# Kernel tuning notes

Measured on AMD Instinct MI355X. Metric: run time of the kernel, lower is better.

The kernel has to match this reference:

```python
import jax, jax.numpy as jnp
import numpy as np

L, B, S, D, H, FF = 6, 4, 1024, 256, 8, 128
DH = D // H
EPS = 1e-5


def _ln(x, w, b):
    m = x.mean(-1, keepdims=True)
    v = ((x - m) ** 2).mean(-1, keepdims=True)
    return (x - m) / jnp.sqrt(v + EPS) * w + b


def setup_inputs() -> dict:
    key = jax.random.key(0)
    ks = jax.random.split(key, 6)
    s = lambda k, shape: jax.random.normal(k, shape, jnp.float32) * 0.02
    return {
        "x": jax.random.normal(ks[0], (B, S, D), jnp.float32),
        "ln1_w": jnp.ones((L, D), jnp.float32),
        "ln1_b": jnp.zeros((L, D), jnp.float32),
        "wqkv": s(ks[1], (L, D, 3 * D)),   # qkv_linear, bias=False
        "wout": s(ks[2], (L, D, D)),       # out_linear, bias=False
        "ln2_w": jnp.ones((L, D), jnp.float32),
        "ln2_b": jnp.zeros((L, D), jnp.float32),
        "w1": s(ks[3], (L, D, 2 * FF)),    # Linear(d_model, 2*ff)
        "b1": jnp.zeros((L, 2 * FF), jnp.float32),
        "w2": s(ks[4], (L, FF, D)),        # Linear(ff, d_model)
        "b2": jnp.zeros((L, D), jnp.float32),
    }


def reference(x, ln1_w, ln1_b, wqkv, wout, ln2_w, ln2_b, w1, b1, w2, b2):
    attn_weights_list = []
    scale = 1.0 / jnp.sqrt(jnp.float32(DH))
    for i in range(L):
        # --- pre-norm multi-head attention ---
        xn = _ln(x, ln1_w[i], ln1_b[i])
        qkv = xn @ wqkv[i]                       # [B,S,3D]
        q, k, v = jnp.split(qkv, 3, axis=-1)
        rs = lambda t: t.reshape(B, S, H, DH).transpose(0, 2, 1, 3)  # b h s d
        q, k, v = rs(q), rs(k), rs(v)
        logits = jnp.einsum('bhid,bhjd->bhij', q, k) * scale
        aw = jax.nn.softmax(logits, axis=-1)     # [B,H,S,S] (dropout=0, eval)
        attn_weights_list.append(aw)
        o = jnp.einsum('bhij,bhjd->bhid', aw, v)
        o = o.transpose(0, 2, 1, 3).reshape(B, S, D) @ wout[i]
        x = x + o
        # --- pre-norm GEGLU FFN ---
        h = _ln(x, ln2_w[i], ln2_b[i]) @ w1[i] + b1[i]   # [B,S,2*FF]
        a, g = jnp.split(h, 2, axis=-1)
        x = x + (a * jax.nn.gelu(g, approximate=False)) @ w2[i] + b2[i]
    return x, jnp.stack(attn_weights_list)      # [B,S,D], [L,B,H,S,S]
```

## Files before the change

kernel.cpp:

```cpp
#include <hip/hip_runtime.h>
#include <hip/hip_bf16.h>

typedef __bf16 bf16x8 __attribute__((ext_vector_type(8)));
typedef __bf16 bf16x4 __attribute__((ext_vector_type(4)));
typedef float  f32x4  __attribute__((ext_vector_type(4)));

#define LAYERS 6
#define BATCH  4
#define SEQ    1024
#define DMODEL 256
#define NHEAD  8
#define DHEAD  32
#define FFDIM  128
#define ROWS   (BATCH*SEQ)
#define QKVN   (3*DMODEL)
#define QSCALE 0.2550348616f

static __device__ __forceinline__ bf16x8 ldg8(const __bf16* p) {
  return *reinterpret_cast<const bf16x8*>(p);
}
#define MFMA16(a, b, c) __builtin_amdgcn_mfma_f32_16x16x32_bf16((a), (b), (c), 0, 0, 0)

__global__ void k_prep(const float* __restrict__ wqkv, const float* __restrict__ wout,
                       const float* __restrict__ w1, const float* __restrict__ w2,
                       __bf16* __restrict__ wqkvT, __bf16* __restrict__ woutT,
                       __bf16* __restrict__ w1T, __bf16* __restrict__ w2T) {
  const int N1 = LAYERS * DMODEL * QKVN;
  const int N2 = LAYERS * DMODEL * DMODEL;
  const int N3 = LAYERS * DMODEL * 2 * FFDIM;
  const int N4 = LAYERS * FFDIM * DMODEL;
  int total = N1 + N2 + N3 + N4;
  for (int i = blockIdx.x * blockDim.x + threadIdx.x; i < total; i += gridDim.x * blockDim.x) {
    int j = i;
    if (j < N1) {
      int l = j / (DMODEL * QKVN), rc = j - l * (DMODEL * QKVN);
      int r = rc / QKVN, c = rc - r * QKVN;
      wqkvT[(size_t)l * DMODEL * QKVN + (size_t)c * DMODEL + r] = (__bf16)wqkv[j]; continue;
    } j -= N1;
    if (j < N2) {
      int l = j / (DMODEL * DMODEL), rc = j - l * (DMODEL * DMODEL);
      int r = rc / DMODEL, c = rc - r * DMODEL;
      woutT[(size_t)l * DMODEL * DMODEL + (size_t)c * DMODEL + r] = (__bf16)wout[j]; continue;
    } j -= N2;
    if (j < N3) {
      int l = j / (DMODEL * 2 * FFDIM), rc = j - l * (DMODEL * 2 * FFDIM);
      int r = rc / (2 * FFDIM), c = rc - r * (2 * FFDIM);
      w1T[(size_t)l * DMODEL * 2 * FFDIM + (size_t)c * DMODEL + r] = (__bf16)w1[j]; continue;
    } j -= N3;
    {
      int l = j / (FFDIM * DMODEL), rc = j - l * (FFDIM * DMODEL);
      int r = rc / DMODEL, c = rc - r * DMODEL;
      w2T[(size_t)l * FFDIM * DMODEL + (size_t)c * FFDIM + r] = (__bf16)w2[j];
    }
  }
}

__global__ __launch_bounds__(64) void k_ln(const float* __restrict__ x,
                                           const float* __restrict__ w,
                                           const float* __restrict__ b,
                                           __bf16* __restrict__ out) {
  int row = blockIdx.x, l = threadIdx.x;
  const float* xr = x + (size_t)row * DMODEL;
  float v[4];
  #pragma unroll
  for (int j = 0; j < 4; ++j) v[j] = xr[l + 64 * j];
  float s = v[0] + v[1] + v[2] + v[3];
  #pragma unroll
  for (int off = 32; off >= 1; off >>= 1) s += __shfl_xor(s, off);
  float mean = s * (1.0f / DMODEL);
  float sq = 0.f;
  #pragma unroll
  for (int j = 0; j < 4; ++j) { v[j] -= mean; sq += v[j] * v[j]; }
  #pragma unroll
  for (int off = 32; off >= 1; off >>= 1) sq += __shfl_xor(sq, off);
  float rstd = rsqrtf(sq * (1.0f / DMODEL) + 1e-5f);
  __bf16* orow = out + (size_t)row * DMODEL;
  #pragma unroll
  for (int j = 0; j < 4; ++j) {
    int c = l + 64 * j;
    orow[c] = (__bf16)(v[j] * rstd * w[c] + b[c]);
  }
}

__global__ __launch_bounds__(256) void k_qkv(const __bf16* __restrict__ xn,
                                             const __bf16* __restrict__ Bt,
                                             __bf16* __restrict__ qb,
                                             __bf16* __restrict__ kt,
                                             __bf16* __restrict__ vt) {
  int w = threadIdx.x >> 6, l = threadIdx.x & 63, lr = l & 15, lg = l >> 4;
  int m0 = blockIdx.x * 64 + w * 16;
  int n0 = blockIdx.y * 64;
  f32x4 acc[4] = {};
  const __bf16* ap = xn + (size_t)(m0 + lr) * DMODEL + 8 * lg;
  const __bf16* bp = Bt + (size_t)(n0 + lr) * DMODEL + 8 * lg;
  for (int kc = 0; kc < DMODEL; kc += 32) {
    bf16x8 a = ldg8(ap + kc);
    #pragma unroll
    for (int t = 0; t < 4; ++t) {
      bf16x8 b = ldg8(bp + (size_t)t * 16 * DMODEL + kc);
      acc[t] = MFMA16(a, b, acc[t]);
    }
  }
  int row = m0 + lg * 4;
  if (n0 < DMODEL) {
    #pragma unroll
    for (int t = 0; t < 4; ++t) {
      int col = n0 + t * 16 + lr;
      #pragma unroll
      for (int r = 0; r < 4; ++r)
        qb[(size_t)(row + r) * DMODEL + col] = (__bf16)(acc[t][r] * QSCALE);
    }
  } else if (n0 < 2 * DMODEL) {
    int b_ = row >> 10, s = row & (SEQ - 1);
    #pragma unroll
    for (int t = 0; t < 4; ++t) {
      int hdh = n0 - DMODEL + t * 16 + lr;
      int h = hdh >> 5, dh = hdh & 31;
      size_t base = ((size_t)(b_ * NHEAD + h) * SEQ + s) * DHEAD + dh;
      #pragma unroll
      for (int r = 0; r < 4; ++r) kt[base + (size_t)r * DHEAD] = (__bf16)acc[t][r];
    }
  } else {
    int b_ = row >> 10, s = row & (SEQ - 1);
    #pragma unroll
    for (int t = 0; t < 4; ++t) {
      int hdh = n0 - 2 * DMODEL + t * 16 + lr;
      int h = hdh >> 5, dh = hdh & 31;
      bf16x4 v4;
      #pragma unroll
      for (int r = 0; r < 4; ++r) v4[r] = (__bf16)acc[t][r];
      *reinterpret_cast<bf16x4*>(vt + ((size_t)(b_ * NHEAD + h) * DHEAD + dh) * SEQ + s) = v4;
    }
  }
}

__global__ __launch_bounds__(512, 6) void k_attn(const __bf16* __restrict__ qb,
                                                 const __bf16* __restrict__ kt,
                                                 const __bf16* __restrict__ vt,
                                                 __bf16* __restrict__ ob,
                                                 float* __restrict__ aw) {
  __shared__ __bf16 P[8][2][16][40];
  __shared__ float  Ssum[8][16];
  __shared__ float  OS[8][16][34];
  int bid = blockIdx.x;
  int swz = (bid & 7) * 256 + (bid >> 3);
  int qblk = swz & 63, h = (swz >> 6) & 7, b = swz >> 9;
  int w = threadIdx.x >> 6, l = threadIdx.x & 63, lr = l & 15, lg = l >> 4;
  int q0 = qblk * 16;
  bf16x8 qf = ldg8(qb + ((size_t)(b * SEQ) + q0 + lr) * DMODEL + h * DHEAD + 8 * lg);
  const __bf16* ktb = kt + (size_t)(b * NHEAD + h) * SEQ * DHEAD + 8 * lg;
  const __bf16* vtb = vt + (size_t)(b * NHEAD + h) * DHEAD * SEQ;
  f32x4 z = {};
  int kbeg = w * 128;

  float s4[4] = {0.f, 0.f, 0.f, 0.f};
  #pragma unroll 4
  for (int t = 0; t < 8; ++t) {
    bf16x8 kf = ldg8(ktb + (size_t)(kbeg + t * 16 + lr) * DHEAD);
    f32x4 d = MFMA16(qf, kf, z);
    #pragma unroll
    for (int r = 0; r < 4; ++r) s4[r] += exp2f(d[r]);
  }
  #pragma unroll
  for (int off = 1; off < 16; off <<= 1) {
    #pragma unroll
    for (int r = 0; r < 4; ++r) s4[r] += __shfl_xor(s4[r], off);
  }
  if (lr == 0) {
    #pragma unroll
    for (int r = 0; r < 4; ++r) Ssum[w][lg * 4 + r] = s4[r];
  }
  __syncthreads();
  float rinv[4];
  #pragma unroll
  for (int r = 0; r < 4; ++r) {
    int row = lg * 4 + r;
    float s = Ssum[0][row] + Ssum[1][row] + Ssum[2][row] + Ssum[3][row]
            + Ssum[4][row] + Ssum[5][row] + Ssum[6][row] + Ssum[7][row];
    rinv[r] = 1.0f / s;
  }

  float* awb = aw + ((size_t)(b * NHEAD + h) * SEQ) * SEQ;
  float (*ST)[32] = reinterpret_cast<float(*)[32]>(&OS[w][0][0]);

#define QK_TILE(KC, BUF)                                                          \
  {                                                                               \
    _Pragma("unroll")                                                             \
    for (int half = 0; half < 2; ++half) {                                        \
      int k0 = (KC) + half * 16;                                                  \
      bf16x8 kf = ldg8(ktb + (size_t)(k0 + lr) * DHEAD);                          \
      f32x4 d = MFMA16(qf, kf, z);                                                \
      _Pragma("unroll")                                                           \
      for (int r = 0; r < 4; ++r) {                                               \
        float pn = exp2f(d[r]) * rinv[r];                                         \
        ST[lg * 4 + r][half * 16 + lr] = pn;                                      \
        P[w][BUF][lg * 4 + r][half * 16 + lr] = (__bf16)pn;                       \
      }                                                                           \
    }                                                                             \
  }

#define FLUSH(KC)                                                                 \
  {                                                                               \
    int frow = l >> 3, fcol = (l & 7) * 4;                                        \
    f32x4 v0 = *reinterpret_cast<const f32x4*>(&ST[frow][fcol]);                  \
    f32x4 v1 = *reinterpret_cast<const f32x4*>(&ST[frow + 8][fcol]);              \
    __builtin_nontemporal_store(v0, reinterpret_cast<f32x4*>(                     \
        &awb[(size_t)(q0 + frow) * SEQ + (KC) + fcol]));                          \
    __builtin_nontemporal_store(v1, reinterpret_cast<f32x4*>(                     \
        &awb[(size_t)(q0 + frow + 8) * SEQ + (KC) + fcol]));                      \
  }

  f32x4 accO[2] = {};
  QK_TILE(kbeg, 0)
  #pragma unroll
  for (int j = 1; j < 4; ++j) {
    int kc = kbeg + j * 32;
    bf16x8 pf  = *reinterpret_cast<const bf16x8*>(&P[w][(j - 1) & 1][lr][8 * lg]);
    bf16x8 vf0 = ldg8(vtb + (size_t)lr * SEQ + (kc - 32) + 8 * lg);
    bf16x8 vf1 = ldg8(vtb + (size_t)(16 + lr) * SEQ + (kc - 32) + 8 * lg);
    FLUSH(kc - 32)
    QK_TILE(kc, j & 1)
    accO[0] = MFMA16(pf, vf0, accO[0]);
    accO[1] = MFMA16(pf, vf1, accO[1]);
  }
  {
    bf16x8 pf  = *reinterpret_cast<const bf16x8*>(&P[w][1][lr][8 * lg]);
    bf16x8 vf0 = ldg8(vtb + (size_t)lr * SEQ + (kbeg + 96) + 8 * lg);
    bf16x8 vf1 = ldg8(vtb + (size_t)(16 + lr) * SEQ + (kbeg + 96) + 8 * lg);
    FLUSH(kbeg + 96)
    accO[0] = MFMA16(pf, vf0, accO[0]);
    accO[1] = MFMA16(pf, vf1, accO[1]);
  }
#undef QK_TILE
#undef FLUSH

  #pragma unroll
  for (int t = 0; t < 2; ++t)
    #pragma unroll
    for (int r = 0; r < 4; ++r) OS[w][lg * 4 + r][t * 16 + lr] = accO[t][r];
  __syncthreads();
  int row = threadIdx.x >> 5, col = threadIdx.x & 31;
  float o = 0.f;
  #pragma unroll
  for (int ww = 0; ww < 8; ++ww) o += OS[ww][row][col];
  ob[((size_t)(b * SEQ) + q0 + row) * DMODEL + h * DHEAD + col] = (__bf16)o;
}

template <int LAST>
__global__ __launch_bounds__(512) void k_pf(const __bf16* __restrict__ ob,
                                            const __bf16* __restrict__ woutT,
                                            const float* __restrict__ xres,
                                            const float* __restrict__ ln2w,
                                            const float* __restrict__ ln2b,
                                            const __bf16* __restrict__ w1t,
                                            const float* __restrict__ b1,
                                            const __bf16* __restrict__ w2t,
                                            const float* __restrict__ b2,
                                            float* __restrict__ x32out,
                                            const float* __restrict__ lnw_n,
                                            const float* __restrict__ lnb_n,
                                            const __bf16* __restrict__ wqkvT_n,
                                            __bf16* __restrict__ qb,
                                            __bf16* __restrict__ kt,
                                            __bf16* __restrict__ vt,
                                            float* __restrict__ xout) {
  __shared__ float  xs[16][268];
  __shared__ __bf16 XN[16][264];
  __shared__ __bf16 G[16][136];
  __shared__ __bf16 HT[16][136];
  int w = threadIdx.x >> 6, l = threadIdx.x & 63, lr = l & 15, lg = l >> 4;
  int m0 = blockIdx.x * 16;
  {
    int n0 = w * 32;
    f32x4 acc[2] = {};
    const __bf16* ap = ob + (size_t)(m0 + lr) * DMODEL + 8 * lg;
    const __bf16* bp = woutT + (size_t)(n0 + lr) * DMODEL + 8 * lg;
    for (int kc = 0; kc < DMODEL; kc += 32) {
      bf16x8 a = ldg8(ap + kc);
      #pragma unroll
      for (int t = 0; t < 2; ++t)
        acc[t] = MFMA16(a, ldg8(bp + (size_t)t * 16 * DMODEL + kc), acc[t]);
    }
    #pragma unroll
    for (int t = 0; t < 2; ++t) {
      int col = n0 + t * 16 + lr;
      #pragma unroll
      for (int r = 0; r < 4; ++r) {
        int row = lg * 4 + r;
        xs[row][col] = acc[t][r] + xres[(size_t)(m0 + row) * DMODEL + col];
      }
    }
  }
  __syncthreads();
  #pragma unroll
  for (int rr = 0; rr < 2; ++rr) {
    int row = w * 2 + rr;
    f32x4 v = *reinterpret_cast<const f32x4*>(&xs[row][4 * l]);
    float s = v[0] + v[1] + v[2] + v[3];
    #pragma unroll
    for (int off = 32; off >= 1; off >>= 1) s += __shfl_xor(s, off);
    float mean = s * (1.0f / DMODEL);
    float sq = 0.f;
    f32x4 c;
    #pragma unroll
    for (int j = 0; j < 4; ++j) { c[j] = v[j] - mean; sq += c[j] * c[j]; }
    #pragma unroll
    for (int off = 32; off >= 1; off >>= 1) sq += __shfl_xor(sq, off);
    float rstd = rsqrtf(sq * (1.0f / DMODEL) + 1e-5f);
    f32x4 lwv = *reinterpret_cast<const f32x4*>(&ln2w[4 * l]);
    f32x4 lbv = *reinterpret_cast<const f32x4*>(&ln2b[4 * l]);
    bf16x4 o4;
    #pragma unroll
    for (int j = 0; j < 4; ++j) o4[j] = (__bf16)(c[j] * rstd * lwv[j] + lbv[j]);
    *reinterpret_cast<bf16x4*>(&XN[row][4 * l]) = o4;
  }
  __syncthreads();
  int n0f = w * 32;
  f32x4 acc1[2] = {};
  {
    const __bf16* bp = w1t + (size_t)(n0f + lr) * DMODEL + 8 * lg;
    for (int kc = 0; kc < DMODEL; kc += 32) {
      bf16x8 a = *reinterpret_cast<const bf16x8*>(&XN[lr][kc + 8 * lg]);
      #pragma unroll
      for (int t = 0; t < 2; ++t)
        acc1[t] = MFMA16(a, ldg8(bp + (size_t)t * 16 * DMODEL + kc), acc1[t]);
    }
  }
  if (w >= 4) {
    #pragma unroll
    for (int t = 0; t < 2; ++t) {
      int col = n0f + t * 16 + lr;
      #pragma unroll
      for (int r = 0; r < 4; ++r) {
        float g = acc1[t][r] + b1[col];
        float ge = 0.5f * g * (1.0f + erff(g * 0.70710678118654752f));
        G[lg * 4 + r][col - 128] = (__bf16)ge;
      }
    }
  }
  __syncthreads();
  if (w < 4) {
    #pragma unroll
    for (int t = 0; t < 2; ++t) {
      int col = n0f + t * 16 + lr;
      #pragma unroll
      for (int r = 0; r < 4; ++r) {
        float a1 = acc1[t][r] + b1[col];
        HT[lg * 4 + r][col] = (__bf16)(a1 * (float)G[lg * 4 + r][col]);
      }
    }
  }
  __syncthreads();
  {
    f32x4 acc2[2] = {};
    const __bf16* bp = w2t + (size_t)(n0f + lr) * FFDIM + 8 * lg;
    for (int kc = 0; kc < FFDIM; kc += 32) {
      bf16x8 a2 = *reinterpret_cast<const bf16x8*>(&HT[lr][kc + 8 * lg]);
      #pragma unroll
      for (int t = 0; t < 2; ++t)
        acc2[t] = MFMA16(a2, ldg8(bp + (size_t)t * 16 * FFDIM + kc), acc2[t]);
    }
    #pragma unroll
    for (int t = 0; t < 2; ++t) {
      int col = n0f + t * 16 + lr;
      #pragma unroll
      for (int r = 0; r < 4; ++r) {
        int row = lg * 4 + r;
        xs[row][col] = acc2[t][r] + b2[col] + xs[row][col];
      }
    }
  }
  __syncthreads();
  #pragma unroll
  for (int rr = 0; rr < 2; ++rr) {
    int row = w * 2 + rr;
    f32x4 v = *reinterpret_cast<const f32x4*>(&xs[row][4 * l]);
    if (LAST) {
      *reinterpret_cast<f32x4*>(&xout[(size_t)(m0 + row) * DMODEL + 4 * l]) = v;
    } else {
      float s = v[0] + v[1] + v[2] + v[3];
      #pragma unroll
      for (int off = 32; off >= 1; off >>= 1) s += __shfl_xor(s, off);
      float mean = s * (1.0f / DMODEL);
      float sq = 0.f;
      f32x4 c;
      #pragma unroll
      for (int j = 0; j < 4; ++j) { c[j] = v[j] - mean; sq += c[j] * c[j]; }
      #pragma unroll
      for (int off = 32; off >= 1; off >>= 1) sq += __shfl_xor(sq, off);
      float rstd = rsqrtf(sq * (1.0f / DMODEL) + 1e-5f);
      *reinterpret_cast<f32x4*>(&x32out[(size_t)(m0 + row) * DMODEL + 4 * l]) = v;
      f32x4 lwv = *reinterpret_cast<const f32x4*>(&lnw_n[4 * l]);
      f32x4 lbv = *reinterpret_cast<const f32x4*>(&lnb_n[4 * l]);
      bf16x4 o4;
      #pragma unroll
      for (int j = 0; j < 4; ++j) o4[j] = (__bf16)(c[j] * rstd * lwv[j] + lbv[j]);
      *reinterpret_cast<bf16x4*>(&XN[row][4 * l]) = o4;
    }
  }
  if (!LAST) {
    __syncthreads();
    f32x4 acc[6] = {};
    {
      const __bf16* bp = wqkvT_n + (size_t)(w * 96 + lr) * DMODEL + 8 * lg;
      for (int kc = 0; kc < DMODEL; kc += 32) {
        bf16x8 a = *reinterpret_cast<const bf16x8*>(&XN[lr][kc + 8 * lg]);
        #pragma unroll
        for (int t = 0; t < 6; ++t)
          acc[t] = MFMA16(a, ldg8(bp + (size_t)t * 16 * DMODEL + kc), acc[t]);
      }
    }
    int row = m0 + lg * 4;
    int b_ = row >> 10, s = row & (SEQ - 1);
    #pragma unroll
    for (int t = 0; t < 6; ++t) {
      int col = w * 96 + t * 16 + lr;
      if (col < DMODEL) {
        #pragma unroll
        for (int r = 0; r < 4; ++r)
          qb[(size_t)(row + r) * DMODEL + col] = (__bf16)(acc[t][r] * QSCALE);
      } else if (col < 2 * DMODEL) {
        int hdh = col - DMODEL;
        int h = hdh >> 5, dh = hdh & 31;
        size_t base = ((size_t)(b_ * NHEAD + h) * SEQ + s) * DHEAD + dh;
        #pragma unroll
        for (int r = 0; r < 4; ++r) kt[base + (size_t)r * DHEAD] = (__bf16)acc[t][r];
      } else {
        int hdh = col - 2 * DMODEL;
        int h = hdh >> 5, dh = hdh & 31;
        bf16x4 v4;
        #pragma unroll
        for (int r = 0; r < 4; ++r) v4[r] = (__bf16)acc[t][r];
        *reinterpret_cast<bf16x4*>(vt + ((size_t)(b_ * NHEAD + h) * DHEAD + dh) * SEQ + s) = v4;
      }
    }
  }
}

static inline size_t align256(size_t x) { return (x + 255) & ~(size_t)255; }

extern "C" void kernel_launch(void* const* d_in, const int* in_sizes, int n_in,
                              void* d_out, int out_size, void* d_ws, size_t ws_size,
                              hipStream_t stream) {
  const float* x_in = (const float*)d_in[0];
  const float* ln1w = (const float*)d_in[1];
  const float* ln1b = (const float*)d_in[2];
  const float* wqkv = (const float*)d_in[3];
  const float* wout = (const float*)d_in[4];
  const float* ln2w = (const float*)d_in[5];
  const float* ln2b = (const float*)d_in[6];
  const float* w1   = (const float*)d_in[7];
  const float* b1   = (const float*)d_in[8];
  const float* w2   = (const float*)d_in[9];
  const float* b2   = (const float*)d_in[10];
  float* out = (float*)d_out;

  char* p = (char*)d_ws;
  float*  x32   = (float*)p;  p += align256((size_t)ROWS * DMODEL * 4);
  __bf16* xn    = (__bf16*)p; p += align256((size_t)ROWS * DMODEL * 2);
  __bf16* qb    = (__bf16*)p; p += align256((size_t)ROWS * DMODEL * 2);
  __bf16* kt    = (__bf16*)p; p += align256((size_t)ROWS * DMODEL * 2);
  __bf16* vt    = (__bf16*)p; p += align256((size_t)ROWS * DMODEL * 2);
  __bf16* ob    = (__bf16*)p; p += align256((size_t)ROWS * DMODEL * 2);
  __bf16* wqkvT = (__bf16*)p; p += align256((size_t)LAYERS * DMODEL * QKVN * 2);
  __bf16* woutT = (__bf16*)p; p += align256((size_t)LAYERS * DMODEL * DMODEL * 2);
  __bf16* w1T   = (__bf16*)p; p += align256((size_t)LAYERS * DMODEL * 2 * FFDIM * 2);
  __bf16* w2T   = (__bf16*)p; p += align256((size_t)LAYERS * FFDIM * DMODEL * 2);

  k_prep<<<2048, 256, 0, stream>>>(wqkv, wout, w1, w2, wqkvT, woutT, w1T, w2T);
  k_ln<<<ROWS, 64, 0, stream>>>(x_in, ln1w, ln1b, xn);
  k_qkv<<<dim3(ROWS / 64, QKVN / 64), 256, 0, stream>>>(xn, wqkvT, qb, kt, vt);

  const size_t AW_LAYER = (size_t)BATCH * NHEAD * SEQ * SEQ;
  for (int i = 0; i < LAYERS; ++i) {
    float* aw_l = out + (size_t)ROWS * DMODEL + (size_t)i * AW_LAYER;
    k_attn<<<SEQ / 16 * NHEAD * BATCH, 512, 0, stream>>>(qb, kt, vt, ob, aw_l);
    const float* xres = (i == 0) ? x_in : x32;
    if (i < LAYERS - 1) {
      k_pf<0><<<ROWS / 16, 512, 0, stream>>>(
          ob, woutT + (size_t)i * DMODEL * DMODEL, xres,
          ln2w + i * DMODEL, ln2b + i * DMODEL,
          w1T + (size_t)i * DMODEL * 2 * FFDIM, b1 + i * 2 * FFDIM,
          w2T + (size_t)i * FFDIM * DMODEL, b2 + i * DMODEL,
          x32, ln1w + (i + 1) * DMODEL, ln1b + (i + 1) * DMODEL,
          wqkvT + (size_t)(i + 1) * DMODEL * QKVN, qb, kt, vt, nullptr);
    } else {
      k_pf<1><<<ROWS / 16, 512, 0, stream>>>(
          ob, woutT + (size_t)i * DMODEL * DMODEL, xres,
          ln2w + i * DMODEL, ln2b + i * DMODEL,
          w1T + (size_t)i * DMODEL * 2 * FFDIM, b1 + i * 2 * FFDIM,
          w2T + (size_t)i * FFDIM * DMODEL, b2 + i * DMODEL,
          x32, nullptr, nullptr, nullptr, nullptr, nullptr, nullptr, out);
    }
  }
}
```

Baseline: 428.1 us.

## Tile weight transpose via shared memory, pair GEGLU halves per wave, use plain stores

```diff
diff --git a/kernel.cpp b/kernel.cpp
--- a/kernel.cpp
+++ b/kernel.cpp
@@ -21,37 +21,24 @@
 }
 #define MFMA16(a, b, c) __builtin_amdgcn_mfma_f32_16x16x32_bf16((a), (b), (c), 0, 0, 0)
 
-__global__ void k_prep(const float* __restrict__ wqkv, const float* __restrict__ wout,
-                       const float* __restrict__ w1, const float* __restrict__ w2,
-                       __bf16* __restrict__ wqkvT, __bf16* __restrict__ woutT,
-                       __bf16* __restrict__ w1T, __bf16* __restrict__ w2T) {
-  const int N1 = LAYERS * DMODEL * QKVN;
-  const int N2 = LAYERS * DMODEL * DMODEL;
-  const int N3 = LAYERS * DMODEL * 2 * FFDIM;
-  const int N4 = LAYERS * FFDIM * DMODEL;
-  int total = N1 + N2 + N3 + N4;
-  for (int i = blockIdx.x * blockDim.x + threadIdx.x; i < total; i += gridDim.x * blockDim.x) {
-    int j = i;
-    if (j < N1) {
-      int l = j / (DMODEL * QKVN), rc = j - l * (DMODEL * QKVN);
-      int r = rc / QKVN, c = rc - r * QKVN;
-      wqkvT[(size_t)l * DMODEL * QKVN + (size_t)c * DMODEL + r] = (__bf16)wqkv[j]; continue;
-    } j -= N1;
-    if (j < N2) {
-      int l = j / (DMODEL * DMODEL), rc = j - l * (DMODEL * DMODEL);
-      int r = rc / DMODEL, c = rc - r * DMODEL;
-      woutT[(size_t)l * DMODEL * DMODEL + (size_t)c * DMODEL + r] = (__bf16)wout[j]; continue;
-    } j -= N2;
-    if (j < N3) {
-      int l = j / (DMODEL * 2 * FFDIM), rc = j - l * (DMODEL * 2 * FFDIM);
-      int r = rc / (2 * FFDIM), c = rc - r * (2 * FFDIM);
-      w1T[(size_t)l * DMODEL * 2 * FFDIM + (size_t)c * DMODEL + r] = (__bf16)w1[j]; continue;
-    } j -= N3;
-    {
-      int l = j / (FFDIM * DMODEL), rc = j - l * (FFDIM * DMODEL);
-      int r = rc / DMODEL, c = rc - r * DMODEL;
-      w2T[(size_t)l * FFDIM * DMODEL + (size_t)c * FFDIM + r] = (__bf16)w2[j];
-    }
+__global__ __launch_bounds__(256) void k_prepT(const float* __restrict__ in,
+                                               __bf16* __restrict__ out,
+                                               int R, int C) {
+  __shared__ __bf16 T[64][72];
+  int l = blockIdx.z, r0 = blockIdx.y * 64, c0 = blockIdx.x * 64;
+  const float* src = in + ((size_t)l * R + r0) * C + c0;
+  int tr = threadIdx.x >> 6, tc = threadIdx.x & 63;
+  #pragma unroll 4
+  for (int it = 0; it < 16; ++it) {
+    int r = it * 4 + tr;
+    T[r][tc] = (__bf16)src[(size_t)r * C + tc];
+  }
+  __syncthreads();
+  __bf16* dst = out + ((size_t)l * C + c0) * R + r0;
+  #pragma unroll 4
+  for (int it = 0; it < 16; ++it) {
+    int c = it * 4 + tr;
+    dst[(size_t)c * R + tc] = T[tc][c];
   }
 }
 
@@ -204,10 +191,8 @@
     int frow = l >> 3, fcol = (l & 7) * 4;                                        \
     f32x4 v0 = *reinterpret_cast<const f32x4*>(&ST[frow][fcol]);                  \
     f32x4 v1 = *reinterpret_cast<const f32x4*>(&ST[frow + 8][fcol]);              \
-    __builtin_nontemporal_store(v0, reinterpret_cast<f32x4*>(                     \
-        &awb[(size_t)(q0 + frow) * SEQ + (KC) + fcol]));                          \
-    __builtin_nontemporal_store(v1, reinterpret_cast<f32x4*>(                     \
-        &awb[(size_t)(q0 + frow + 8) * SEQ + (KC) + fcol]));                      \
+    *reinterpret_cast<f32x4*>(&awb[(size_t)(q0 + frow) * SEQ + (KC) + fcol]) = v0;\
+    *reinterpret_cast<f32x4*>(&awb[(size_t)(q0 + frow + 8) * SEQ + (KC) + fcol]) = v1;\
   }
 
   f32x4 accO[2] = {};
@@ -266,7 +251,6 @@
                                             float* __restrict__ xout) {
   __shared__ float  xs[16][268];
   __shared__ __bf16 XN[16][264];
-  __shared__ __bf16 G[16][136];
   __shared__ __bf16 HT[16][136];
   int w = threadIdx.x >> 6, l = threadIdx.x & 63, lr = l & 15, lg = l >> 4;
   int m0 = blockIdx.x * 16;
@@ -315,45 +299,29 @@
     *reinterpret_cast<bf16x4*>(&XN[row][4 * l]) = o4;
   }
   __syncthreads();
-  int n0f = w * 32;
-  f32x4 acc1[2] = {};
   {
-    const __bf16* bp = w1t + (size_t)(n0f + lr) * DMODEL + 8 * lg;
+    f32x4 acc1[2] = {};
+    const __bf16* bpa = w1t + (size_t)(w * 16 + lr) * DMODEL + 8 * lg;
+    const __bf16* bpg = w1t + (size_t)(128 + w * 16 + lr) * DMODEL + 8 * lg;
     for (int kc = 0; kc < DMODEL; kc += 32) {
       bf16x8 a = *reinterpret_cast<const bf16x8*>(&XN[lr][kc + 8 * lg]);
-      #pragma unroll
-      for (int t = 0; t < 2; ++t)
-        acc1[t] = MFMA16(a, ldg8(bp + (size_t)t * 16 * DMODEL + kc), acc1[t]);
-    }
-  }
-  if (w >= 4) {
-    #pragma unroll
-    for (int t = 0; t < 2; ++t) {
-      int col = n0f + t * 16 + lr;
-      #pragma unroll
-      for (int r = 0; r < 4; ++r) {
-        float g = acc1[t][r] + b1[col];
-        float ge = 0.5f * g * (1.0f + erff(g * 0.70710678118654752f));
-        G[lg * 4 + r][col - 128] = (__bf16)ge;
-      }
-    }
-  }
-  __syncthreads();
-  if (w < 4) {
-    #pragma unroll
-    for (int t = 0; t < 2; ++t) {
-      int col = n0f + t * 16 + lr;
-      #pragma unroll
-      for (int r = 0; r < 4; ++r) {
-        float a1 = acc1[t][r] + b1[col];
-        HT[lg * 4 + r][col] = (__bf16)(a1 * (float)G[lg * 4 + r][col]);
-      }
+      acc1[0] = MFMA16(a, ldg8(bpa + kc), acc1[0]);
+      acc1[1] = MFMA16(a, ldg8(bpg + kc), acc1[1]);
+    }
+    int fc = w * 16 + lr;
+    #pragma unroll
+    for (int r = 0; r < 4; ++r) {
+      float a1 = acc1[0][r] + b1[fc];
+      float g  = acc1[1][r] + b1[fc + 128];
+      float ge = 0.5f * g * (1.0f + erff(g * 0.70710678118654752f));
+      HT[lg * 4 + r][fc] = (__bf16)(a1 * ge);
     }
   }
   __syncthreads();
   {
+    int n0 = w * 32;
     f32x4 acc2[2] = {};
-    const __bf16* bp = w2t + (size_t)(n0f + lr) * FFDIM + 8 * lg;
+    const __bf16* bp = w2t + (size_t)(n0 + lr) * FFDIM + 8 * lg;
     for (int kc = 0; kc < FFDIM; kc += 32) {
       bf16x8 a2 = *reinterpret_cast<const bf16x8*>(&HT[lr][kc + 8 * lg]);
       #pragma unroll
@@ -362,7 +330,7 @@
     }
     #pragma unroll
     for (int t = 0; t < 2; ++t) {
-      int col = n0f + t * 16 + lr;
+      int col = n0 + t * 16 + lr;
       #pragma unroll
       for (int r = 0; r < 4; ++r) {
         int row = lg * 4 + r;
@@ -467,7 +435,10 @@
   __bf16* w1T   = (__bf16*)p; p += align256((size_t)LAYERS * DMODEL * 2 * FFDIM * 2);
   __bf16* w2T   = (__bf16*)p; p += align256((size_t)LAYERS * FFDIM * DMODEL * 2);
 
-  k_prep<<<2048, 256, 0, stream>>>(wqkv, wout, w1, w2, wqkvT, woutT, w1T, w2T);
+  k_prepT<<<dim3(QKVN / 64, DMODEL / 64, LAYERS), 256, 0, stream>>>(wqkv, wqkvT, DMODEL, QKVN);
+  k_prepT<<<dim3(DMODEL / 64, DMODEL / 64, LAYERS), 256, 0, stream>>>(wout, woutT, DMODEL, DMODEL);
+  k_prepT<<<dim3(2 * FFDIM / 64, DMODEL / 64, LAYERS), 256, 0, stream>>>(w1, w1T, DMODEL, 2 * FFDIM);
+  k_prepT<<<dim3(DMODEL / 64, FFDIM / 64, LAYERS), 256, 0, stream>>>(w2, w2T, FFDIM, DMODEL);
   k_ln<<<ROWS, 64, 0, stream>>>(x_in, ln1w, ln1b, xn);
   k_qkv<<<dim3(ROWS / 64, QKVN / 64), 256, 0, stream>>>(xn, wqkvT, qb, kt, vt);
 
```

Result: slower. 444.7 us (+3.9%).
